# Optimization experiments

Measured on AMD Instinct MI355X. Metric: run time of the kernel, lower is better.

Reference implementation:

```python
import jax, jax.numpy as jnp
import numpy as np

N_ENT = 2000
GAT_EMB = 64
GAT_HID = 3
HIDDEN = 256
BATCH = 8
ALPHA = 0.2  # LeakyReLU negative slope
MASK_FILL = jnp.float32(9e-15)  # original fills masked-out logits with 9e-15 (NOT -inf)


def setup_inputs() -> dict:
    key = jax.random.key(0)
    k1, k2, k3, k4, k5, k6 = jax.random.split(key, 6)
    emb = jax.random.normal(k1, (N_ENT, GAT_EMB), dtype=jnp.float32)
    W = jax.random.normal(k2, (GAT_EMB, GAT_HID), dtype=jnp.float32) * 0.2
    a = jax.random.normal(k3, (2 * GAT_HID, 1), dtype=jnp.float32) * 0.2
    fc1_w = jax.random.normal(k4, (HIDDEN, N_ENT * GAT_HID), dtype=jnp.float32) * 0.02
    fc1_b = jax.random.normal(k5, (HIDDEN,), dtype=jnp.float32) * 0.02
    adj = jax.random.randint(k6, (BATCH, N_ENT, N_ENT), 0, 2, dtype=jnp.int32)
    return {"emb": emb, "W": W, "a": a, "fc1_w": fc1_w, "fc1_b": fc1_b, "adj": adj}


def reference(emb, W, a, fc1_w, fc1_b, adj):
    # h = emb @ W : [N, 3] -- shared across all graphs in the batch
    h = emb @ W
    # Pairwise logits: original concatenates [h_i, h_j] and dots with a;
    # equivalent to (h @ a1)_i + (h @ a2)_j via broadcasting (no O(N^2*2H) tensor).
    s1 = h @ a[:GAT_HID, 0]   # [N]
    s2 = h @ a[GAT_HID:, 0]   # [N]
    e = jax.nn.leaky_relu(s1[:, None] + s2[None, :], negative_slope=ALPHA)  # [N, N]
    # Mask by adjacency (fill 9e-15, matching original), softmax over neighbors (dim=1)
    masked = jnp.where(adj > 0, e[None, :, :], MASK_FILL)  # [B, N, N]
    att = jax.nn.softmax(masked, axis=2)
    # Weighted aggregation + ELU (concat=True head)
    h_prime = jnp.einsum('bij,jd->bid', att, h)  # [B, N, 3]
    x = jax.nn.elu(h_prime).reshape(att.shape[0], -1)  # [B, N*3]
    return x @ fc1_w.T + fc1_b  # [B, hidden]
```

## Files before the change

### kernel.cpp

```cpp
#include <hip/hip_runtime.h>
#include <cstddef>

#define N_ENT   2000
#define NPAD    2048
#define GAT_EMB 64
#define GAT_HID 3
#define HIDDEN  256
#define BATCH   8
#define ALPHA   0.2f

#define WS_BYTES  40960

__global__ __launch_bounds__(256) void k_init(const float* __restrict__ fc1_b,
                                              float* __restrict__ out) {
    int idx = blockIdx.x * 256 + threadIdx.x;
    out[idx] = fc1_b[idx & (HIDDEN - 1)];
}

__global__ __launch_bounds__(256) void k_prep(const float* __restrict__ emb,
                                              const float* __restrict__ W,
                                              const float* __restrict__ a,
                                              float* __restrict__ ws) {
    __shared__ float sW[GAT_EMB * GAT_HID];
    __shared__ float sa[2 * GAT_HID];
    int t = threadIdx.x;
    if (t < GAT_EMB * GAT_HID) sW[t] = W[t];
    if (t < 2 * GAT_HID)       sa[t] = a[t];
    __syncthreads();
    int i = blockIdx.x * 256 + t;
    if (i >= N_ENT) return;
    const float4* er = (const float4*)(emb + (size_t)i * GAT_EMB);
    float h0 = 0.f, h1 = 0.f, h2 = 0.f;
#pragma unroll
    for (int k4 = 0; k4 < GAT_EMB / 4; ++k4) {
        float4 e4 = er[k4];
        int k = 4 * k4;
        h0 += e4.x * sW[(k + 0) * 3 + 0]; h1 += e4.x * sW[(k + 0) * 3 + 1]; h2 += e4.x * sW[(k + 0) * 3 + 2];
        h0 += e4.y * sW[(k + 1) * 3 + 0]; h1 += e4.y * sW[(k + 1) * 3 + 1]; h2 += e4.y * sW[(k + 1) * 3 + 2];
        h0 += e4.z * sW[(k + 2) * 3 + 0]; h1 += e4.z * sW[(k + 2) * 3 + 1]; h2 += e4.z * sW[(k + 2) * 3 + 2];
        h0 += e4.w * sW[(k + 3) * 3 + 0]; h1 += e4.w * sW[(k + 3) * 3 + 1]; h2 += e4.w * sW[(k + 3) * 3 + 2];
    }
    ws[0 * NPAD + i] = h0 * sa[3] + h1 * sa[4] + h2 * sa[5];
    ws[1 * NPAD + i] = h0;
    ws[2 * NPAD + i] = h1;
    ws[3 * NPAD + i] = h2;
    ws[4 * NPAD + i] = h0 * sa[0] + h1 * sa[1] + h2 * sa[2];
}

__global__ __launch_bounds__(256) void k_main(const float* __restrict__ emb,
                                              const float* __restrict__ W,
                                              const float* __restrict__ a,
                                              const float* __restrict__ fc1_w,
                                              const int*   __restrict__ adj,
                                              const float* __restrict__ wsrc,
                                              int use_ws,
                                              float* __restrict__ out) {
    __shared__ __align__(16) float s2s[NPAD];
    __shared__ __align__(16) float h0s[NPAD];
    __shared__ __align__(16) float h1s[NPAD];
    __shared__ __align__(16) float h2s[NPAD];
    __shared__ float sW[GAT_EMB * GAT_HID];
    __shared__ float sa[2 * GAT_HID];
    __shared__ float s1_own[4];
    __shared__ float xblk[BATCH][16];

    int t  = threadIdx.x;
    int i0 = blockIdx.x * 4;

    if (use_ws) {
        const float4* s = (const float4*)wsrc;
        for (int idx = t; idx < N_ENT / 4; idx += 256) {
            ((float4*)s2s)[idx] = s[0 * (NPAD / 4) + idx];
            ((float4*)h0s)[idx] = s[1 * (NPAD / 4) + idx];
            ((float4*)h1s)[idx] = s[2 * (NPAD / 4) + idx];
            ((float4*)h2s)[idx] = s[3 * (NPAD / 4) + idx];
        }
        if (t < 4) s1_own[t] = wsrc[4 * NPAD + i0 + t];
    } else {
        if (t < GAT_EMB * GAT_HID) sW[t] = W[t];
        if (t < 2 * GAT_HID)       sa[t] = a[t];
        __syncthreads();
        for (int j = t; j < N_ENT; j += 256) {
            const float4* er = (const float4*)(emb + (size_t)j * GAT_EMB);
            float h0 = 0.f, h1 = 0.f, h2 = 0.f;
#pragma unroll
            for (int k4 = 0; k4 < GAT_EMB / 4; ++k4) {
                float4 e4 = er[k4];
                int k = 4 * k4;
                h0 += e4.x * sW[(k + 0) * 3 + 0]; h1 += e4.x * sW[(k + 0) * 3 + 1]; h2 += e4.x * sW[(k + 0) * 3 + 2];
                h0 += e4.y * sW[(k + 1) * 3 + 0]; h1 += e4.y * sW[(k + 1) * 3 + 1]; h2 += e4.y * sW[(k + 1) * 3 + 2];
                h0 += e4.z * sW[(k + 2) * 3 + 0]; h1 += e4.z * sW[(k + 2) * 3 + 1]; h2 += e4.z * sW[(k + 2) * 3 + 2];
                h0 += e4.w * sW[(k + 3) * 3 + 0]; h1 += e4.w * sW[(k + 3) * 3 + 1]; h2 += e4.w * sW[(k + 3) * 3 + 2];
            }
            s2s[j] = h0 * sa[3] + h1 * sa[4] + h2 * sa[5];
            h0s[j] = h0; h1s[j] = h1; h2s[j] = h2;
            if (j >= i0 && j < i0 + 4)
                s1_own[j - i0] = h0 * sa[0] + h1 * sa[1] + h2 * sa[2];
        }
    }
    __syncthreads();

    int lane = t & 63;
    int w    = t >> 6;
    int i    = i0 + w;
    float s1v = s1_own[w];
    const int* __restrict__ base = adj + (size_t)i * N_ENT;

    float acc[BATCH][4];
#pragma unroll
    for (int b = 0; b < BATCH; ++b) { acc[b][0] = 0.f; acc[b][1] = 0.f; acc[b][2] = 0.f; acc[b][3] = 0.f; }

#pragma unroll 1
    for (int k = 0; k < (N_ENT + 255) / 256; ++k) {
        int j0 = k * 256 + lane * 4;
        if (j0 < N_ENT) {
            int4 m[BATCH];
#pragma unroll
            for (int b = 0; b < BATCH; ++b)
                m[b] = *(const int4*)(base + (size_t)b * (N_ENT * N_ENT) + j0);
            float4 s2v = *(const float4*)&s2s[j0];
            float4 h0v = *(const float4*)&h0s[j0];
            float4 h1v = *(const float4*)&h1s[j0];
            float4 h2v = *(const float4*)&h2s[j0];
            float ev[4];
#pragma unroll
            for (int q = 0; q < 4; ++q) {
                float e  = s1v + ((const float*)&s2v)[q];
                float lr = fmaxf(e, 0.f) + ALPHA * fminf(e, 0.f);
                ev[q] = __expf(lr);
            }
#pragma unroll
            for (int b = 0; b < BATCH; ++b) {
                const int* mb = (const int*)&m[b];
#pragma unroll
                for (int q = 0; q < 4; ++q) {
                    float e = (mb[q] > 0) ? ev[q] : 1.0f;
                    acc[b][0] += e;
                    acc[b][1] += e * ((const float*)&h0v)[q];
                    acc[b][2] += e * ((const float*)&h1v)[q];
                    acc[b][3] += e * ((const float*)&h2v)[q];
                }
            }
        }
    }

#pragma unroll
    for (int off = 32; off > 0; off >>= 1)
#pragma unroll
        for (int b = 0; b < BATCH; ++b) {
            acc[b][0] += __shfl_xor(acc[b][0], off, 64);
            acc[b][1] += __shfl_xor(acc[b][1], off, 64);
            acc[b][2] += __shfl_xor(acc[b][2], off, 64);
            acc[b][3] += __shfl_xor(acc[b][3], off, 64);
        }

    if (lane == 0) {
#pragma unroll
        for (int b = 0; b < BATCH; ++b) {
            float inv = 1.f / acc[b][0];
            float p0 = acc[b][1] * inv, p1 = acc[b][2] * inv, p2 = acc[b][3] * inv;
            xblk[b][3 * w + 0] = (p0 > 0.f) ? p0 : expm1f(p0);
            xblk[b][3 * w + 1] = (p1 > 0.f) ? p1 : expm1f(p1);
            xblk[b][3 * w + 2] = (p2 > 0.f) ? p2 : expm1f(p2);
        }
    }
    __syncthreads();

    {
        int k = t;
        const float4* wr4 = (const float4*)(fc1_w + (size_t)k * (N_ENT * GAT_HID) + 3 * i0);
        float4 wa = wr4[0], wb = wr4[1], wc = wr4[2];
#pragma unroll
        for (int b = 0; b < BATCH; ++b) {
            float d = xblk[b][0]  * wa.x + xblk[b][1]  * wa.y + xblk[b][2]  * wa.z + xblk[b][3]  * wa.w
                    + xblk[b][4]  * wb.x + xblk[b][5]  * wb.y + xblk[b][6]  * wb.z + xblk[b][7]  * wb.w
                    + xblk[b][8]  * wc.x + xblk[b][9]  * wc.y + xblk[b][10] * wc.z + xblk[b][11] * wc.w;
            atomicAdd(&out[b * HIDDEN + k], d);
        }
    }
}

extern "C" void kernel_launch(void* const* d_in, const int* in_sizes, int n_in,
                              void* d_out, int out_size, void* d_ws, size_t ws_size,
                              hipStream_t stream) {
    const float* emb   = (const float*)d_in[0];
    const float* W     = (const float*)d_in[1];
    const float* a     = (const float*)d_in[2];
    const float* fc1_w = (const float*)d_in[3];
    const float* fc1_b = (const float*)d_in[4];
    const int*   adj   = (const int*)d_in[5];
    float* out = (float*)d_out;
    float* ws  = (float*)d_ws;

    int use_ws = (ws_size >= (size_t)WS_BYTES) ? 1 : 0;
    k_init<<<8, 256, 0, stream>>>(fc1_b, out);
    if (use_ws) k_prep<<<8, 256, 0, stream>>>(emb, W, a, ws);
    k_main<<<N_ENT / 4, 256, 0, stream>>>(emb, W, a, fc1_w, adj, ws, use_ws, out);
}
```

Measured before the change: 218.0 us.

## Split rows across batch-halves, fp16 h tables, and separate FC kernel without atomics

The main kernel now processes 2 rows per block, with each wave handling one row and half of the batch. This raises the block count and cuts per-thread accumulator state, and launch bounds request higher occupancy. The h tables are stored as fp16 to halve shared-memory footprint and staging traffic. When the workspace is large enough, the ELU outputs are written to workspace as fp16, and a separate k_fc kernel does the fc1 GEMV with bias, replacing the many global atomics. The fp16 conversion of h and x adds precision loss.

```diff
diff --git a/kernel.cpp b/kernel.cpp
--- a/kernel.cpp
+++ b/kernel.cpp
@@ -2,14 +2,20 @@
 #include <cstddef>
 
 #define N_ENT   2000
-#define NPAD    2048
 #define GAT_EMB 64
-#define GAT_HID 3
 #define HIDDEN  256
 #define BATCH   8
 #define ALPHA   0.2f
 
-#define WS_BYTES  40960
+typedef _Float16 half4 __attribute__((ext_vector_type(4)));
+
+#define WS_HX_OFF      8192
+#define WS_HY_OFF      12288
+#define WS_HZ_OFF      16384
+#define WS_S1_OFF      20480
+#define WS_TABLE_BYTES 28672
+#define WS_X_OFF       28672
+#define WS_TIER2_BYTES 124672
 
 __global__ __launch_bounds__(256) void k_init(const float* __restrict__ fc1_b,
                                               float* __restrict__ out) {
@@ -21,11 +27,11 @@
                                               const float* __restrict__ W,
                                               const float* __restrict__ a,
                                               float* __restrict__ ws) {
-    __shared__ float sW[GAT_EMB * GAT_HID];
-    __shared__ float sa[2 * GAT_HID];
+    __shared__ float sW[GAT_EMB * 3];
+    __shared__ float sa[6];
     int t = threadIdx.x;
-    if (t < GAT_EMB * GAT_HID) sW[t] = W[t];
-    if (t < 2 * GAT_HID)       sa[t] = a[t];
+    if (t < GAT_EMB * 3) sW[t] = W[t];
+    if (t < 6)           sa[t] = a[t];
     __syncthreads();
     int i = blockIdx.x * 256 + t;
     if (i >= N_ENT) return;
@@ -40,45 +46,43 @@
         h0 += e4.z * sW[(k + 2) * 3 + 0]; h1 += e4.z * sW[(k + 2) * 3 + 1]; h2 += e4.z * sW[(k + 2) * 3 + 2];
         h0 += e4.w * sW[(k + 3) * 3 + 0]; h1 += e4.w * sW[(k + 3) * 3 + 1]; h2 += e4.w * sW[(k + 3) * 3 + 2];
     }
-    ws[0 * NPAD + i] = h0 * sa[3] + h1 * sa[4] + h2 * sa[5];
-    ws[1 * NPAD + i] = h0;
-    ws[2 * NPAD + i] = h1;
-    ws[3 * NPAD + i] = h2;
-    ws[4 * NPAD + i] = h0 * sa[0] + h1 * sa[1] + h2 * sa[2];
-}
-
-__global__ __launch_bounds__(256) void k_main(const float* __restrict__ emb,
-                                              const float* __restrict__ W,
-                                              const float* __restrict__ a,
-                                              const float* __restrict__ fc1_w,
-                                              const int*   __restrict__ adj,
-                                              const float* __restrict__ wsrc,
-                                              int use_ws,
-                                              float* __restrict__ out) {
-    __shared__ __align__(16) float s2s[NPAD];
-    __shared__ __align__(16) float h0s[NPAD];
-    __shared__ __align__(16) float h1s[NPAD];
-    __shared__ __align__(16) float h2s[NPAD];
-    __shared__ float sW[GAT_EMB * GAT_HID];
-    __shared__ float sa[2 * GAT_HID];
-    __shared__ float s1_own[4];
-    __shared__ float xblk[BATCH][16];
+    ws[i] = h0 * sa[3] + h1 * sa[4] + h2 * sa[5];
+    ((_Float16*)((char*)ws + WS_HX_OFF))[i] = (_Float16)h0;
+    ((_Float16*)((char*)ws + WS_HY_OFF))[i] = (_Float16)h1;
+    ((_Float16*)((char*)ws + WS_HZ_OFF))[i] = (_Float16)h2;
+    ws[WS_S1_OFF / 4 + i] = h0 * sa[0] + h1 * sa[1] + h2 * sa[2];
+}
+
+__global__ __launch_bounds__(256, 4) void k_main(const float* __restrict__ emb,
+                                                 const float* __restrict__ W,
+                                                 const float* __restrict__ a,
+                                                 const float* __restrict__ fc1_w,
+                                                 const int*   __restrict__ adj,
+                                                 float* __restrict__ wsf,
+                                                 int mode,
+                                                 float* __restrict__ out) {
+    __shared__ __align__(16) unsigned char smem[20480];
+    float*    s2s = (float*)smem;
+    _Float16* hxs = (_Float16*)(smem + 8192);
+    _Float16* hys = (_Float16*)(smem + 12288);
+    _Float16* hzs = (_Float16*)(smem + 16384);
+    __shared__ float sW[GAT_EMB * 3];
+    __shared__ float sa[6];
+    __shared__ float s1sh[2];
+    __shared__ float xblk[BATCH][8];
 
     int t  = threadIdx.x;
-    int i0 = blockIdx.x * 4;
-
-    if (use_ws) {
-        const float4* s = (const float4*)wsrc;
-        for (int idx = t; idx < N_ENT / 4; idx += 256) {
-            ((float4*)s2s)[idx] = s[0 * (NPAD / 4) + idx];
-            ((float4*)h0s)[idx] = s[1 * (NPAD / 4) + idx];
-            ((float4*)h1s)[idx] = s[2 * (NPAD / 4) + idx];
-            ((float4*)h2s)[idx] = s[3 * (NPAD / 4) + idx];
-        }
-        if (t < 4) s1_own[t] = wsrc[4 * NPAD + i0 + t];
+    int g  = blockIdx.x;
+    int i0 = g * 2;
+
+    if (mode != 0) {
+        const uint4* src = (const uint4*)wsf;
+        uint4* dst = (uint4*)smem;
+#pragma unroll
+        for (int rep = 0; rep < 5; ++rep) dst[rep * 256 + t] = src[rep * 256 + t];
     } else {
-        if (t < GAT_EMB * GAT_HID) sW[t] = W[t];
-        if (t < 2 * GAT_HID)       sa[t] = a[t];
+        if (t < GAT_EMB * 3) sW[t] = W[t];
+        if (t < 6)           sa[t] = a[t];
         __syncthreads();
         for (int j = t; j < N_ENT; j += 256) {
             const float4* er = (const float4*)(emb + (size_t)j * GAT_EMB);
@@ -93,90 +97,154 @@
                 h0 += e4.w * sW[(k + 3) * 3 + 0]; h1 += e4.w * sW[(k + 3) * 3 + 1]; h2 += e4.w * sW[(k + 3) * 3 + 2];
             }
             s2s[j] = h0 * sa[3] + h1 * sa[4] + h2 * sa[5];
-            h0s[j] = h0; h1s[j] = h1; h2s[j] = h2;
-            if (j >= i0 && j < i0 + 4)
-                s1_own[j - i0] = h0 * sa[0] + h1 * sa[1] + h2 * sa[2];
-        }
+            hxs[j] = (_Float16)h0; hys[j] = (_Float16)h1; hzs[j] = (_Float16)h2;
+            if (j == i0 || j == i0 + 1)
+                s1sh[j - i0] = h0 * sa[0] + h1 * sa[1] + h2 * sa[2];
+        }
+    }
+    if (t < 2048 - N_ENT) {
+        int j = N_ENT + t;
+        s2s[j] = 0.f; hxs[j] = (_Float16)0; hys[j] = (_Float16)0; hzs[j] = (_Float16)0;
     }
     __syncthreads();
 
     int lane = t & 63;
     int w    = t >> 6;
-    int i    = i0 + w;
-    float s1v = s1_own[w];
-    const int* __restrict__ base = adj + (size_t)i * N_ENT;
-
-    float acc[BATCH][4];
-#pragma unroll
-    for (int b = 0; b < BATCH; ++b) { acc[b][0] = 0.f; acc[b][1] = 0.f; acc[b][2] = 0.f; acc[b][3] = 0.f; }
+    int di   = w >> 1;
+    int b0   = (w & 1) * 4;
+    int i    = i0 + di;
+    float s1v = (mode == 0) ? s1sh[di] : wsf[WS_S1_OFF / 4 + i];
+
+    const int* __restrict__ bp[4];
+    float ac0[4], ac1[4], ac2[4], ac3[4];
+#pragma unroll
+    for (int s = 0; s < 4; ++s) {
+        bp[s] = adj + ((size_t)(b0 + s) * N_ENT + i) * N_ENT;
+        ac0[s] = 0.f; ac1[s] = 0.f; ac2[s] = 0.f; ac3[s] = 0.f;
+    }
 
 #pragma unroll 1
-    for (int k = 0; k < (N_ENT + 255) / 256; ++k) {
-        int j0 = k * 256 + lane * 4;
-        if (j0 < N_ENT) {
-            int4 m[BATCH];
-#pragma unroll
-            for (int b = 0; b < BATCH; ++b)
-                m[b] = *(const int4*)(base + (size_t)b * (N_ENT * N_ENT) + j0);
-            float4 s2v = *(const float4*)&s2s[j0];
-            float4 h0v = *(const float4*)&h0s[j0];
-            float4 h1v = *(const float4*)&h1s[j0];
-            float4 h2v = *(const float4*)&h2s[j0];
-            float ev[4];
+    for (int kk = 0; kk < 4; ++kk) {
+        int jA = kk * 512 + (lane << 2);
+        int jB = jA + 256;
+        bool pB = (jB < N_ENT);
+        int jBs = pB ? jB : 0;
+        int4 mA[4], mB[4];
+#pragma unroll
+        for (int s = 0; s < 4; ++s) mA[s] = *(const int4*)(bp[s] + jA);
+#pragma unroll
+        for (int s = 0; s < 4; ++s) mB[s] = *(const int4*)(bp[s] + jBs);
+
+        float4 s2A = *(const float4*)&s2s[jA];
+        float4 s2B = *(const float4*)&s2s[jB];
+        half4  hxA = *(const half4*)&hxs[jA], hxB = *(const half4*)&hxs[jB];
+        half4  hyA = *(const half4*)&hys[jA], hyB = *(const half4*)&hys[jB];
+        half4  hzA = *(const half4*)&hzs[jA], hzB = *(const half4*)&hzs[jB];
+
+        float evA[4], evB[4], hAx[4], hAy[4], hAz[4], hBx[4], hBy[4], hBz[4];
+#pragma unroll
+        for (int q = 0; q < 4; ++q) {
+            float e = s1v + ((const float*)&s2A)[q];
+            evA[q] = __expf(fmaxf(e, 0.f) + ALPHA * fminf(e, 0.f));
+            float f = s1v + ((const float*)&s2B)[q];
+            evB[q] = __expf(fmaxf(f, 0.f) + ALPHA * fminf(f, 0.f));
+            hAx[q] = (float)hxA[q]; hAy[q] = (float)hyA[q]; hAz[q] = (float)hzA[q];
+            hBx[q] = (float)hxB[q]; hBy[q] = (float)hyB[q]; hBz[q] = (float)hzB[q];
+        }
+        float zB = pB ? 1.0f : 0.0f;
+#pragma unroll
+        for (int s = 0; s < 4; ++s) {
+            const int* ma = (const int*)&mA[s];
+            const int* mb = (const int*)&mB[s];
 #pragma unroll
             for (int q = 0; q < 4; ++q) {
-                float e  = s1v + ((const float*)&s2v)[q];
-                float lr = fmaxf(e, 0.f) + ALPHA * fminf(e, 0.f);
-                ev[q] = __expf(lr);
+                float eA = (ma[q] > 0) ? evA[q] : 1.0f;
+                ac0[s] += eA; ac1[s] += eA * hAx[q]; ac2[s] += eA * hAy[q]; ac3[s] += eA * hAz[q];
+                float eB = ((mb[q] > 0) ? evB[q] : 1.0f) * zB;
+                ac0[s] += eB; ac1[s] += eB * hBx[q]; ac2[s] += eB * hBy[q]; ac3[s] += eB * hBz[q];
             }
-#pragma unroll
-            for (int b = 0; b < BATCH; ++b) {
-                const int* mb = (const int*)&m[b];
-#pragma unroll
-                for (int q = 0; q < 4; ++q) {
-                    float e = (mb[q] > 0) ? ev[q] : 1.0f;
-                    acc[b][0] += e;
-                    acc[b][1] += e * ((const float*)&h0v)[q];
-                    acc[b][2] += e * ((const float*)&h1v)[q];
-                    acc[b][3] += e * ((const float*)&h2v)[q];
-                }
+        }
+    }
+
+#pragma unroll
+    for (int off = 32; off > 0; off >>= 1)
+#pragma unroll
+        for (int s = 0; s < 4; ++s) {
+            ac0[s] += __shfl_xor(ac0[s], off, 64);
+            ac1[s] += __shfl_xor(ac1[s], off, 64);
+            ac2[s] += __shfl_xor(ac2[s], off, 64);
+            ac3[s] += __shfl_xor(ac3[s], off, 64);
+        }
+
+    if (lane == 0) {
+#pragma unroll
+        for (int s = 0; s < 4; ++s) {
+            float inv = 1.f / ac0[s];
+            float p0 = ac1[s] * inv, p1 = ac2[s] * inv, p2 = ac3[s] * inv;
+            xblk[b0 + s][3 * di + 0] = (p0 > 0.f) ? p0 : expm1f(p0);
+            xblk[b0 + s][3 * di + 1] = (p1 > 0.f) ? p1 : expm1f(p1);
+            xblk[b0 + s][3 * di + 2] = (p2 > 0.f) ? p2 : expm1f(p2);
+        }
+    }
+    __syncthreads();
+
+    if (mode == 2) {
+        if (t < 48) {
+            int b = t & 7, c = t >> 3;
+            _Float16* x16 = (_Float16*)((char*)wsf + WS_X_OFF);
+            x16[(size_t)(6 * g + c) * 8 + b] = (_Float16)xblk[b][c];
+        }
+    } else {
+        int k = (t + g * 19) & 255;
+        const float* wr = fc1_w + (size_t)k * (N_ENT * 3) + 6 * g;
+        float2 wA = *(const float2*)wr;
+        float2 wB = *(const float2*)(wr + 2);
+        float2 wC = *(const float2*)(wr + 4);
+#pragma unroll
+        for (int b = 0; b < BATCH; ++b) {
+            float d = xblk[b][0] * wA.x + xblk[b][1] * wA.y
+                    + xblk[b][2] * wB.x + xblk[b][3] * wB.y
+                    + xblk[b][4] * wC.x + xblk[b][5] * wC.y;
+            atomicAdd(&out[b * HIDDEN + k], d);
+        }
+    }
+}
+
+__global__ __launch_bounds__(256) void k_fc(const _Float16* __restrict__ x16,
+                                            const float* __restrict__ fc1_w,
+                                            const float* __restrict__ fc1_b,
+                                            float* __restrict__ out) {
+    int t = threadIdx.x, lane = t & 63, w = t >> 6;
+    int k = blockIdx.x * 4 + w;
+    const float* __restrict__ wr = fc1_w + (size_t)k * (N_ENT * 3);
+    float acc[BATCH];
+#pragma unroll
+    for (int b = 0; b < BATCH; ++b) acc[b] = 0.f;
+#pragma unroll 1
+    for (int it = 0; it < 24; ++it) {
+        int m0 = it * 256 + (lane << 2);
+        if (m0 < N_ENT * 3) {
+            float4 wv4 = *(const float4*)(wr + m0);
+#pragma unroll
+            for (int q = 0; q < 4; ++q) {
+                half4 xa = *(const half4*)(x16 + (size_t)(m0 + q) * 8);
+                half4 xb = *(const half4*)(x16 + (size_t)(m0 + q) * 8 + 4);
+                float wv = ((const float*)&wv4)[q];
+                acc[0] += wv * (float)xa[0]; acc[1] += wv * (float)xa[1];
+                acc[2] += wv * (float)xa[2]; acc[3] += wv * (float)xa[3];
+                acc[4] += wv * (float)xb[0]; acc[5] += wv * (float)xb[1];
+                acc[6] += wv * (float)xb[2]; acc[7] += wv * (float)xb[3];
             }
         }
     }
-
 #pragma unroll
     for (int off = 32; off > 0; off >>= 1)
 #pragma unroll
-        for (int b = 0; b < BATCH; ++b) {
-            acc[b][0] += __shfl_xor(acc[b][0], off, 64);
-            acc[b][1] += __shfl_xor(acc[b][1], off, 64);
-            acc[b][2] += __shfl_xor(acc[b][2], off, 64);
-            acc[b][3] += __shfl_xor(acc[b][3], off, 64);
-        }
-
+        for (int b = 0; b < BATCH; ++b) acc[b] += __shfl_xor(acc[b], off, 64);
     if (lane == 0) {
-#pragma unroll
-        for (int b = 0; b < BATCH; ++b) {
-            float inv = 1.f / acc[b][0];
-            float p0 = acc[b][1] * inv, p1 = acc[b][2] * inv, p2 = acc[b][3] * inv;
-            xblk[b][3 * w + 0] = (p0 > 0.f) ? p0 : expm1f(p0);
-            xblk[b][3 * w + 1] = (p1 > 0.f) ? p1 : expm1f(p1);
-            xblk[b][3 * w + 2] = (p2 > 0.f) ? p2 : expm1f(p2);
-        }
-    }
-    __syncthreads();
-
-    {
-        int k = t;
-        const float4* wr4 = (const float4*)(fc1_w + (size_t)k * (N_ENT * GAT_HID) + 3 * i0);
-        float4 wa = wr4[0], wb = wr4[1], wc = wr4[2];
-#pragma unroll
-        for (int b = 0; b < BATCH; ++b) {
-            float d = xblk[b][0]  * wa.x + xblk[b][1]  * wa.y + xblk[b][2]  * wa.z + xblk[b][3]  * wa.w
-                    + xblk[b][4]  * wb.x + xblk[b][5]  * wb.y + xblk[b][6]  * wb.z + xblk[b][7]  * wb.w
-                    + xblk[b][8]  * wc.x + xblk[b][9]  * wc.y + xblk[b][10] * wc.z + xblk[b][11] * wc.w;
-            atomicAdd(&out[b * HIDDEN + k], d);
-        }
+        float bias = fc1_b[k];
+#pragma unroll
+        for (int b = 0; b < BATCH; ++b) out[b * HIDDEN + k] = acc[b] + bias;
     }
 }
 
@@ -191,9 +259,15 @@
     const int*   adj   = (const int*)d_in[5];
     float* out = (float*)d_out;
     float* ws  = (float*)d_ws;
-
-    int use_ws = (ws_size >= (size_t)WS_BYTES) ? 1 : 0;
-    k_init<<<8, 256, 0, stream>>>(fc1_b, out);
-    if (use_ws) k_prep<<<8, 256, 0, stream>>>(emb, W, a, ws);
-    k_main<<<N_ENT / 4, 256, 0, stream>>>(emb, W, a, fc1_w, adj, ws, use_ws, out);
-}
+    (void)in_sizes; (void)n_in; (void)out_size;
+
+    int tier = (ws_size >= (size_t)WS_TIER2_BYTES) ? 2
+             : (ws_size >= (size_t)WS_TABLE_BYTES) ? 1 : 0;
+
+    if (tier < 2)  k_init<<<8, 256, 0, stream>>>(fc1_b, out);
+    if (tier >= 1) k_prep<<<8, 256, 0, stream>>>(emb, W, a, ws);
+    k_main<<<N_ENT / 2, 256, 0, stream>>>(emb, W, a, fc1_w, adj, ws, tier, out);
+    if (tier == 2)
+        k_fc<<<64, 256, 0, stream>>>((const _Float16*)((char*)d_ws + WS_X_OFF),
+                                     fc1_w, fc1_b, out);
+}
```

Result: slower. 226.0 us (+3.7%).
